# Performance work log

Measured on AMD Instinct MI355X. Metric: run time of the kernel, lower is better.

## Reference

```python
import jax, jax.numpy as jnp
import numpy as np

NEG_SLOPE = 0.2

def gat_conv(x, src, dst, n, W, a_src, a_dst, b):
    # PyG GATConv, heads=1: h = xW; e_ij = LeakyReLU(a_src.h_j + a_dst.h_i)
    # alpha = softmax over incoming edges of i; out_i = sum_j alpha_ij * h_j + b
    h = x @ W                               # [N, F_out]
    s_src = h @ a_src                       # [N]
    s_dst = h @ a_dst                       # [N]
    e = s_src[src] + s_dst[dst]             # [E]
    e = jnp.where(e > 0, e, NEG_SLOPE * e)  # leaky relu
    # numerically stable scatter-softmax over destination groups
    m = jax.ops.segment_max(e, dst, num_segments=n)          # [N]
    ee = jnp.exp(e - m[dst])                                  # [E]
    denom = jax.ops.segment_sum(ee, dst, num_segments=n)      # [N]
    alpha = ee / denom[dst]                                    # [E]
    out = jax.ops.segment_sum(alpha[:, None] * h[src], dst, num_segments=n)
    return out + b

def add_self_loops(edge_index, n):
    loops = jnp.arange(n, dtype=edge_index.dtype)
    src = jnp.concatenate([edge_index[0], loops])
    dst = jnp.concatenate([edge_index[1], loops])
    return src, dst

def setup_inputs() -> dict:
    key = jax.random.key(0)
    ks = jax.random.split(key, 12)
    N, E, F_IN, H1, H2, C = 50000, 800000, 1433, 512, 256, 7
    x = jax.random.normal(ks[0], (N, F_IN), dtype=jnp.float32)
    edge_index = jax.random.randint(ks[1], (2, E), 0, N, dtype=jnp.int64)
    def glorot(k, shape):
        lim = float(np.sqrt(6.0 / (shape[0] + shape[-1])))
        return jax.random.uniform(k, shape, jnp.float32, -lim, lim)
    params = {
        'W1': glorot(ks[2], (F_IN, H1)), 'as1': glorot(ks[3], (H1,)), 'ad1': glorot(ks[4], (H1,)), 'b1': jnp.zeros((H1,), jnp.float32),
        'W2': glorot(ks[5], (H1, H2)), 'as2': glorot(ks[6], (H2,)), 'ad2': glorot(ks[7], (H2,)), 'b2': jnp.zeros((H2,), jnp.float32),
        'W3': glorot(ks[8], (H2, C)), 'as3': glorot(ks[9], (C,)), 'ad3': glorot(ks[10], (C,)), 'b3': jnp.zeros((C,), jnp.float32),
    }
    return {'x': x, 'edge_index': edge_index, **params}

def reference(x, edge_index, W1, as1, ad1, b1, W2, as2, ad2, b2, W3, as3, ad3, b3):
    n = x.shape[0]
    src, dst = add_self_loops(edge_index, n)
    h = jax.nn.relu(gat_conv(x, src, dst, n, W1, as1, ad1, b1))
    h = jax.nn.relu(gat_conv(h, src, dst, n, W2, as2, ad2, b2))
    h = gat_conv(h, src, dst, n, W3, as3, ad3, b3)
    return jax.nn.log_softmax(h, axis=1)
```

## Files before the change

kernel.cpp:

```cpp
#include <hip/hip_runtime.h>
#include <hip/hip_bf16.h>
#include <math.h>

constexpr int N_NODES = 50000;
constexpr int E_EDGES = 800000;
constexpr int E_TOT   = E_EDGES + N_NODES;
constexpr int F_IN  = 1433;
constexpr int KPAD1 = 1440;
constexpr int F1 = 512;
constexpr int F2 = 256;
constexpr int NC = 7;
constexpr int MAXDEG = 1024;
constexpr float NEG_SLOPE = 0.2f;

typedef unsigned short u16;
typedef unsigned int   u32;
typedef short s16x8 __attribute__((ext_vector_type(8)));
typedef float f32x4 __attribute__((ext_vector_type(4)));
typedef float float4a __attribute__((ext_vector_type(4), aligned(4)));

__device__ inline u16 f2b(float f) {
    u32 u = __float_as_uint(f);
    u32 r = (u + 0x7fffu + ((u >> 16) & 1u)) >> 16;
    return (u16)r;
}
__device__ inline float b2f(u16 b) { return __uint_as_float(((u32)b) << 16); }

__device__ inline u32 pkbf16(float lo, float hi) {
    union { __hip_bfloat162 h; u32 u; } c;
    c.h = __float22bfloat162_rn(make_float2(lo, hi));
    return c.u;
}

__device__ inline void gload_lds16(const void* g, void* l) {
    __builtin_amdgcn_global_load_lds(
        (const __attribute__((address_space(1))) u32*)g,
        (__attribute__((address_space(3))) u32*)l, 16, 0, 0);
}

__device__ inline void loadA8_nt(const float* p, int gk, float4a& v0, float4a& v1) {
    if (gk + 8 <= F_IN) {
        v0 = __builtin_nontemporal_load((const float4a*)p);
        v1 = __builtin_nontemporal_load((const float4a*)(p + 4));
    } else {
#pragma unroll
        for (int i = 0; i < 4; ++i) v0[i] = (gk + i < F_IN) ? p[i] : 0.f;
#pragma unroll
        for (int i = 0; i < 4; ++i) v1[i] = (gk + 4 + i < F_IN) ? p[4 + i] : 0.f;
    }
}

__global__ void count_dst_kernel(const int* __restrict__ dst, int* __restrict__ counts) {
    int i = blockIdx.x * blockDim.x + threadIdx.x;
    if (i < E_TOT) {
        int d = (i < E_EDGES) ? dst[i] : (i - E_EDGES);
        atomicAdd(&counts[d], 1);
    }
}

__global__ __launch_bounds__(1024) void scan_kernel(const int* __restrict__ counts,
                                                    int* __restrict__ row_ptr, int n) {
    __shared__ int part[1024];
    int t = threadIdx.x;
    int chunk = (n + 1023) / 1024;
    int lo = t * chunk;
    int hi = min(lo + chunk, n);
    int s = 0;
    for (int i = lo; i < hi; ++i) s += counts[i];
    part[t] = s;
    __syncthreads();
    for (int off = 1; off < 1024; off <<= 1) {
        int v = 0;
        if (t >= off) v = part[t - off];
        __syncthreads();
        part[t] += v;
        __syncthreads();
    }
    int run = part[t] - s;
    for (int i = lo; i < hi; ++i) { row_ptr[i] = run; run += counts[i]; }
    if (t == 1023) row_ptr[n] = part[1023];
}

__global__ void scatter_kernel(const int* __restrict__ src, const int* __restrict__ dst,
                               const int* __restrict__ row_ptr, int* __restrict__ fill,
                               int* __restrict__ col) {
    int i = blockIdx.x * blockDim.x + threadIdx.x;
    if (i < E_TOT) {
        int s = (i < E_EDGES) ? src[i] : (i - E_EDGES);
        int d = (i < E_EDGES) ? dst[i] : (i - E_EDGES);
        int p = row_ptr[d] + atomicAdd(&fill[d], 1);
        col[p] = s;
    }
}

__global__ void convert_wt_kernel(const float* __restrict__ W, u32* __restrict__ Wt,
                                  int K, int Nn, int KP) {
    int p = blockIdx.x * blockDim.x + threadIdx.x;
    int ppr = KP / 2;
    if (p >= Nn * ppr) return;
    int n = p / ppr;
    int k = (p - n * ppr) * 2;
    float v0 = (k + 0 < K) ? W[(size_t)(k + 0) * Nn + n] : 0.f;
    float v1 = (k + 1 < K) ? W[(size_t)(k + 1) * Nn + n] : 0.f;
    Wt[p] = (u32)f2b(v0) | ((u32)f2b(v1) << 16);
}

__global__ __launch_bounds__(256, 2) void gemm1_fused(const float* __restrict__ A,
                                                      const u16* __restrict__ Bt,
                                                      u16* __restrict__ C) {
    constexpr int M = N_NODES;
    constexpr int ABUF = 64 * 32;
    constexpr int BBUF = 512 * 32;
    __shared__ u16 sA[2 * ABUF];
    __shared__ u16 sB[2 * BBUF];
    int tid  = threadIdx.x;
    int wave = tid >> 6;
    int lane = tid & 63;
    int quad = lane >> 4;
    int lm   = lane & 15;
    int m0 = blockIdx.x * 64;

    int arow  = min(m0 + (tid >> 2), M - 1);
    int aslot = (tid & 3) ^ ((tid >> 3) & 3);
    const float* xcol = A + (size_t)arow * F_IN + aslot * 8;
    int acolbase = aslot * 8;

    const u16* gB[8];
    u16* lB[8];
#pragma unroll
    for (int c = 0; c < 8; ++c) {
        int chunk = wave * 8 + c;
        int row  = chunk * 16 + (lane >> 2);
        int slot = (lane & 3) ^ ((lane >> 3) & 3);
        gB[c] = Bt + (size_t)row * KPAD1 + slot * 8;
        lB[c] = &sB[chunk * 512];
    }

    f32x4 acc[4][8];
#pragma unroll
    for (int i = 0; i < 4; ++i)
#pragma unroll
        for (int j = 0; j < 8; ++j) acc[i][j] = (f32x4){0.f, 0.f, 0.f, 0.f};

    int rdoff = (quad ^ ((lm >> 1) & 3)) * 8;

    {
#pragma unroll
        for (int c = 0; c < 8; ++c) gload_lds16(gB[c], lB[c]);
        float4a a0, a1;
        loadA8_nt(xcol, acolbase, a0, a1);
        uint4 pk;
        pk.x = pkbf16(a0[0], a0[1]); pk.y = pkbf16(a0[2], a0[3]);
        pk.z = pkbf16(a1[0], a1[1]); pk.w = pkbf16(a1[2], a1[3]);
        *(uint4*)&sA[tid * 8] = pk;
    }
    __syncthreads();

    int cur = 0;
    for (int k0 = 0; k0 < KPAD1; k0 += 32) {
        int kn = k0 + 32;
        bool hasnext = kn < KPAD1;
        int nxt = cur ^ 1;

        float4a a0, a1;
        if (hasnext) {
#pragma unroll
            for (int c = 0; c < 8; ++c) gload_lds16(gB[c] + kn, lB[c] + nxt * BBUF);
            loadA8_nt(xcol + kn, acolbase + kn, a0, a1);
        }

        const u16* sAc = &sA[cur * ABUF];
        const u16* sBc = &sB[cur * BBUF];
        s16x8 af[4], bf[8];
#pragma unroll
        for (int mt = 0; mt < 4; ++mt)
            af[mt] = *(const s16x8*)&sAc[(mt * 16 + lm) * 32 + rdoff];
#pragma unroll
        for (int nt = 0; nt < 8; ++nt)
            bf[nt] = *(const s16x8*)&sBc[(wave * 128 + nt * 16 + lm) * 32 + rdoff];
#pragma unroll
        for (int mt = 0; mt < 4; ++mt)
#pragma unroll
            for (int nt = 0; nt < 8; ++nt)
                acc[mt][nt] = __builtin_amdgcn_mfma_f32_16x16x32_bf16(
                    af[mt], bf[nt], acc[mt][nt], 0, 0, 0);

        if (hasnext) {
            uint4 pk;
            pk.x = pkbf16(a0[0], a0[1]); pk.y = pkbf16(a0[2], a0[3]);
            pk.z = pkbf16(a1[0], a1[1]); pk.w = pkbf16(a1[2], a1[3]);
            *(uint4*)&sA[nxt * ABUF + tid * 8] = pk;
        }
        __syncthreads();
        cur = nxt;
    }

#pragma unroll
    for (int mt = 0; mt < 4; ++mt) {
        int mbase = m0 + mt * 16 + quad * 4;
#pragma unroll
        for (int nt = 0; nt < 8; ++nt) {
            int n = wave * 128 + nt * 16 + lm;
#pragma unroll
            for (int r = 0; r < 4; ++r) {
                int m = mbase + r;
                if (m < M)
                    __builtin_nontemporal_store(f2b(acc[mt][nt][r]),
                                                &C[(size_t)m * F1 + n]);
            }
        }
    }
}

__global__ __launch_bounds__(256) void mfma_gemm_bt(const u16* __restrict__ A,
                                                    const u16* __restrict__ Bt,
                                                    u16* __restrict__ C,
                                                    int M, int N, int K) {
    __shared__ u16 sA[128 * 32];
    __shared__ u16 sB[128 * 32];
    int tid  = threadIdx.x;
    int wave = tid >> 6;
    int lane = tid & 63;
    int quad = lane >> 4;
    int lm   = lane & 15;
    int wm = wave & 1;
    int wn = wave >> 1;
    int m0 = blockIdx.y * 128;
    int n0 = blockIdx.x * 128;

    int ch0 = wave * 2, ch1 = wave * 2 + 1;
    int rsub = lane >> 2;
    int slot = (lane & 3) ^ ((lane >> 3) & 3);
    int csub = slot * 8;
    int ar0 = min(m0 + ch0 * 16 + rsub, M - 1);
    int ar1 = min(m0 + ch1 * 16 + rsub, M - 1);
    int br0 = n0 + ch0 * 16 + rsub;
    int br1 = n0 + ch1 * 16 + rsub;
    const u16* gA0 = A + (size_t)ar0 * K + csub;
    const u16* gA1 = A + (size_t)ar1 * K + csub;
    const u16* gB0 = Bt + (size_t)br0 * K + csub;
    const u16* gB1 = Bt + (size_t)br1 * K + csub;

    f32x4 acc[4][4];
#pragma unroll
    for (int i = 0; i < 4; ++i)
#pragma unroll
        for (int j = 0; j < 4; ++j) acc[i][j] = (f32x4){0.f, 0.f, 0.f, 0.f};

    int rdoff = (quad ^ ((lm >> 1) & 3)) * 8;

    for (int k0 = 0; k0 < K; k0 += 32) {
        gload_lds16(gA0 + k0, &sA[ch0 * 512]);
        gload_lds16(gA1 + k0, &sA[ch1 * 512]);
        gload_lds16(gB0 + k0, &sB[ch0 * 512]);
        gload_lds16(gB1 + k0, &sB[ch1 * 512]);
        __syncthreads();

        s16x8 af[4], bf[4];
#pragma unroll
        for (int mt = 0; mt < 4; ++mt)
            af[mt] = *(const s16x8*)&sA[(wm * 64 + mt * 16 + lm) * 32 + rdoff];
#pragma unroll
        for (int nt = 0; nt < 4; ++nt)
            bf[nt] = *(const s16x8*)&sB[(wn * 64 + nt * 16 + lm) * 32 + rdoff];
#pragma unroll
        for (int mt = 0; mt < 4; ++mt)
#pragma unroll
            for (int nt = 0; nt < 4; ++nt)
                acc[mt][nt] = __builtin_amdgcn_mfma_f32_16x16x32_bf16(
                    af[mt], bf[nt], acc[mt][nt], 0, 0, 0);
        __syncthreads();
    }

#pragma unroll
    for (int mt = 0; mt < 4; ++mt) {
        int mbase = m0 + wm * 64 + mt * 16 + quad * 4;
#pragma unroll
        for (int nt = 0; nt < 4; ++nt) {
            int n = n0 + wn * 64 + nt * 16 + lm;
#pragma unroll
            for (int r = 0; r < 4; ++r) {
                int m = mbase + r;
                if (m < M) C[(size_t)m * N + n] = f2b(acc[mt][nt][r]);
            }
        }
    }
}

template <int F>
__global__ __launch_bounds__(256) void scores_bf16_kernel(const u16* __restrict__ h,
                                                          const float* __restrict__ a_src,
                                                          const float* __restrict__ a_dst,
                                                          float* __restrict__ s_src,
                                                          float* __restrict__ s_dst, int n) {
    int gwid = (blockIdx.x * blockDim.x + threadIdx.x) >> 6;
    int lane = threadIdx.x & 63;
    if (gwid >= n) return;
    const u32* row = (const u32*)(h + (size_t)gwid * F);
    float acc1 = 0.f, acc2 = 0.f;
    for (int p = lane; p < F / 2; p += 64) {
        u32 u = row[p];
        float v0 = b2f((u16)(u & 0xffff));
        float v1 = b2f((u16)(u >> 16));
        acc1 += v0 * a_src[2 * p] + v1 * a_src[2 * p + 1];
        acc2 += v0 * a_dst[2 * p] + v1 * a_dst[2 * p + 1];
    }
#pragma unroll
    for (int o = 32; o; o >>= 1) {
        acc1 += __shfl_xor(acc1, o);
        acc2 += __shfl_xor(acc2, o);
    }
    if (lane == 0) { s_src[gwid] = acc1; s_dst[gwid] = acc2; }
}

template <int F>
__global__ __launch_bounds__(256) void scores_kernel(const float* __restrict__ h,
                                                     const float* __restrict__ a_src,
                                                     const float* __restrict__ a_dst,
                                                     float* __restrict__ s_src,
                                                     float* __restrict__ s_dst, int n) {
    int gwid = (blockIdx.x * blockDim.x + threadIdx.x) >> 6;
    int lane = threadIdx.x & 63;
    if (gwid >= n) return;
    const float* row = h + (size_t)gwid * F;
    float acc1 = 0.f, acc2 = 0.f;
    for (int f = lane; f < F; f += 64) {
        float v = row[f];
        acc1 += v * a_src[f];
        acc2 += v * a_dst[f];
    }
#pragma unroll
    for (int o = 32; o; o >>= 1) {
        acc1 += __shfl_xor(acc1, o);
        acc2 += __shfl_xor(acc2, o);
    }
    if (lane == 0) { s_src[gwid] = acc1; s_dst[gwid] = acc2; }
}

template <int F, bool OUT_BF16>
__global__ __launch_bounds__(256) void agg_online_kernel(
        const u16* __restrict__ h, const float* __restrict__ s_src,
        const float* __restrict__ s_dst, const float* __restrict__ bias,
        const int* __restrict__ row_ptr, const int* __restrict__ col,
        void* __restrict__ out, int n) {
    constexpr int UPL = F / 128;
    int gwid = (blockIdx.x * blockDim.x + threadIdx.x) >> 6;
    int lane = threadIdx.x & 63;
    if (gwid >= n) return;
    int beg = row_ptr[gwid];
    int end = row_ptr[gwid + 1];
    float sd = s_dst[gwid];
    const u32* hw = (const u32*)h;
    int loff = lane * UPL;

    float m = -1e30f, denom = 0.f;
    float acc[2 * UPL];
#pragma unroll
    for (int e = 0; e < 2 * UPL; ++e) acc[e] = 0.f;

    int j = beg;
    for (; j + 2 <= end; j += 2) {
        int c0 = col[j], c1 = col[j + 1];
        const u32* r0 = hw + (size_t)c0 * (F / 2) + loff;
        const u32* r1 = hw + (size_t)c1 * (F / 2) + loff;
        u32 v0[UPL], v1[UPL];
        if constexpr (UPL == 4) {
            uint4 q0 = *(const uint4*)r0; v0[0]=q0.x; v0[1]=q0.y; v0[2]=q0.z; v0[3]=q0.w;
            uint4 q1 = *(const uint4*)r1; v1[0]=q1.x; v1[1]=q1.y; v1[2]=q1.z; v1[3]=q1.w;
        } else {
            uint2 q0 = *(const uint2*)r0; v0[0]=q0.x; v0[1]=q0.y;
            uint2 q1 = *(const uint2*)r1; v1[0]=q1.x; v1[1]=q1.y;
        }
        float e0 = s_src[c0] + sd; e0 = (e0 > 0.f) ? e0 : NEG_SLOPE * e0;
        float e1 = s_src[c1] + sd; e1 = (e1 > 0.f) ? e1 : NEG_SLOPE * e1;
        float mn = fmaxf(fmaxf(m, e0), e1);
        float sc = expf(m - mn);
        float w0 = expf(e0 - mn);
        float w1 = expf(e1 - mn);
        denom = denom * sc + w0 + w1;
        m = mn;
#pragma unroll
        for (int u = 0; u < UPL; ++u) {
            acc[2*u]   = acc[2*u]   * sc + w0 * b2f((u16)(v0[u] & 0xffff))
                                         + w1 * b2f((u16)(v1[u] & 0xffff));
            acc[2*u+1] = acc[2*u+1] * sc + w0 * b2f((u16)(v0[u] >> 16))
                                         + w1 * b2f((u16)(v1[u] >> 16));
        }
    }
    if (j < end) {
        int c0 = col[j];
        const u32* r0 = hw + (size_t)c0 * (F / 2) + loff;
        u32 v0[UPL];
        if constexpr (UPL == 4) {
            uint4 q0 = *(const uint4*)r0; v0[0]=q0.x; v0[1]=q0.y; v0[2]=q0.z; v0[3]=q0.w;
        } else {
            uint2 q0 = *(const uint2*)r0; v0[0]=q0.x; v0[1]=q0.y;
        }
        float e0 = s_src[c0] + sd; e0 = (e0 > 0.f) ? e0 : NEG_SLOPE * e0;
        float mn = fmaxf(m, e0);
        float sc = expf(m - mn);
        float w0 = expf(e0 - mn);
        denom = denom * sc + w0;
        m = mn;
#pragma unroll
        for (int u = 0; u < UPL; ++u) {
            acc[2*u]   = acc[2*u]   * sc + w0 * b2f((u16)(v0[u] & 0xffff));
            acc[2*u+1] = acc[2*u+1] * sc + w0 * b2f((u16)(v0[u] >> 16));
        }
    }

    float inv = 1.0f / denom;
    if constexpr (OUT_BF16) {
        const float2* bp2 = (const float2*)bias;
        u32 ov[UPL];
#pragma unroll
        for (int u = 0; u < UPL; ++u) {
            float2 bb = bp2[loff + u];
            float v0 = fmaxf(acc[2*u]   * inv + bb.x, 0.f);
            float v1 = fmaxf(acc[2*u+1] * inv + bb.y, 0.f);
            ov[u] = pkbf16(v0, v1);
        }
        u32* op = (u32*)out + (size_t)gwid * (F / 2) + loff;
        if constexpr (UPL == 4) {
            uint4 q = {ov[0], ov[1], ov[2], ov[3]};
            *(uint4*)op = q;
        } else {
            uint2 q = {ov[0], ov[1]};
            *(uint2*)op = q;
        }
    } else {
        const float* bp = bias + 2 * loff;
        float4 q = { fmaxf(acc[0] * inv + bp[0], 0.f),
                     fmaxf(acc[1] * inv + bp[1], 0.f),
                     fmaxf(acc[2] * inv + bp[2], 0.f),
                     fmaxf(acc[3] * inv + bp[3], 0.f) };
        *(float4*)((float*)out + (size_t)gwid * F + 2 * loff) = q;
    }
}

__global__ __launch_bounds__(64) void agg_lsm7_kernel(const float* __restrict__ h,
                                                      const float* __restrict__ s_src,
                                                      const float* __restrict__ s_dst,
                                                      const float* __restrict__ bias,
                                                      const int* __restrict__ row_ptr,
                                                      const int* __restrict__ col,
                                                      float* __restrict__ out) {
    int node = blockIdx.x;
    int lane = threadIdx.x;
    int beg = row_ptr[node];
    int deg = min(row_ptr[node + 1] - beg, MAXDEG);

    __shared__ float w[MAXDEG];
    __shared__ int cs[MAXDEG];

    float sd = s_dst[node];
    float m = -1e30f;
    for (int j = lane; j < deg; j += 64) {
        int s = col[beg + j];
        cs[j] = s;
        float e = s_src[s] + sd;
        e = (e > 0.f) ? e : NEG_SLOPE * e;
        w[j] = e;
        m = fmaxf(m, e);
    }
#pragma unroll
    for (int o = 32; o; o >>= 1) m = fmaxf(m, __shfl_xor(m, o));
    float sum = 0.f;
    for (int j = lane; j < deg; j += 64) {
        float v = expf(w[j] - m);
        w[j] = v;
        sum += v;
    }
#pragma unroll
    for (int o = 32; o; o >>= 1) sum += __shfl_xor(sum, o);
    float inv = 1.0f / sum;

    float a[NC];
#pragma unroll
    for (int f = 0; f < NC; ++f) a[f] = 0.f;
    for (int j = lane; j < deg; j += 64) {
        float wg = w[j] * inv;
        const float* row = h + (size_t)cs[j] * NC;
#pragma unroll
        for (int f = 0; f < NC; ++f) a[f] += wg * row[f];
    }
#pragma unroll
    for (int f = 0; f < NC; ++f)
#pragma unroll
        for (int o = 32; o; o >>= 1) a[f] += __shfl_xor(a[f], o);

    if (lane == 0) {
        float vals[NC];
        float mx = -1e30f;
#pragma unroll
        for (int f = 0; f < NC; ++f) { vals[f] = a[f] + bias[f]; mx = fmaxf(mx, vals[f]); }
        float ssum = 0.f;
#pragma unroll
        for (int f = 0; f < NC; ++f) ssum += expf(vals[f] - mx);
        float lse = mx + logf(ssum);
#pragma unroll
        for (int f = 0; f < NC; ++f) out[(size_t)node * NC + f] = vals[f] - lse;
    }
}

__global__ __launch_bounds__(256) void gemm3_kernel(const float* __restrict__ A,
                                                    const float* __restrict__ W,
                                                    float* __restrict__ out, int n) {
    __shared__ float sW[F2 * NC];
    for (int i = threadIdx.x; i < F2 * NC; i += blockDim.x) sW[i] = W[i];
    __syncthreads();
    int gwid = (blockIdx.x * blockDim.x + threadIdx.x) >> 6;
    int lane = threadIdx.x & 63;
    if (gwid >= n) return;
    const float* row = A + (size_t)gwid * F2;
    float4 v = *(const float4*)(row + lane * 4);
    float res = 0.f;
#pragma unroll
    for (int c = 0; c < NC; ++c) {
        float p = v.x * sW[(lane * 4 + 0) * NC + c] + v.y * sW[(lane * 4 + 1) * NC + c] +
                  v.z * sW[(lane * 4 + 2) * NC + c] + v.w * sW[(lane * 4 + 3) * NC + c];
#pragma unroll
        for (int o = 32; o; o >>= 1) p += __shfl_xor(p, o);
        if (lane == c) res = p;
    }
    if (lane < NC) out[(size_t)gwid * NC + lane] = res;
}

extern "C" void kernel_launch(void* const* d_in, const int* in_sizes, int n_in,
                              void* d_out, int out_size, void* d_ws, size_t ws_size,
                              hipStream_t stream) {
    const float* x   = (const float*)d_in[0];
    const int* ei    = (const int*)d_in[1];
    const int* src   = ei;
    const int* dst   = ei + E_EDGES;
    const float* W1  = (const float*)d_in[2];
    const float* as1 = (const float*)d_in[3];
    const float* ad1 = (const float*)d_in[4];
    const float* b1  = (const float*)d_in[5];
    const float* W2  = (const float*)d_in[6];
    const float* as2 = (const float*)d_in[7];
    const float* ad2 = (const float*)d_in[8];
    const float* b2  = (const float*)d_in[9];
    const float* W3  = (const float*)d_in[10];
    const float* as3 = (const float*)d_in[11];
    const float* ad3 = (const float*)d_in[12];
    const float* b3  = (const float*)d_in[13];
    float* outp = (float*)d_out;

    char* base = (char*)d_ws;
    u16*  a1b = (u16*)base;
    u16*  h2b = (u16*)(base + 51200000);
    float* a2 = (float*)(base + 76800000);
    float* h3 = (float*)(base + 128000000);
    u16*  h1b = (u16*)(base + 144000000);
    u16*  W1t = (u16*)(base + 195200000);
    u16*  W2t = (u16*)(base + 196674560);
    float* ssrc = (float*)(base + 196936704);
    float* sdst = (float*)(base + 197136704);
    int* row_ptr = (int*)(base + 197336704);
    int* counts  = (int*)(base + 197536708);
    int* fill    = (int*)(base + 197736708);
    int* col     = (int*)(base + 197936708);

    hipMemsetAsync(counts, 0, sizeof(int) * N_NODES, stream);
    hipMemsetAsync(fill, 0, sizeof(int) * N_NODES, stream);

    {
        int blk = 256;
        int grid = (E_TOT + blk - 1) / blk;
        count_dst_kernel<<<grid, blk, 0, stream>>>(dst, counts);
        scan_kernel<<<1, 1024, 0, stream>>>(counts, row_ptr, N_NODES);
        scatter_kernel<<<grid, blk, 0, stream>>>(src, dst, row_ptr, fill, col);
    }

    {
        int nw1 = F1 * (KPAD1 / 2);
        convert_wt_kernel<<<(nw1 + 255) / 256, 256, 0, stream>>>(W1, (u32*)W1t, F_IN, F1, KPAD1);
        int nw2 = F2 * (F1 / 2);
        convert_wt_kernel<<<(nw2 + 255) / 256, 256, 0, stream>>>(W2, (u32*)W2t, F1, F2, F1);
    }

    int waves_grid = (N_NODES + 3) / 4;
    int mblocks = (N_NODES + 127) / 128;

    {
        int grid1 = (N_NODES + 63) / 64;
        gemm1_fused<<<grid1, 256, 0, stream>>>(x, W1t, h1b);
        scores_bf16_kernel<F1><<<waves_grid, 256, 0, stream>>>(h1b, as1, ad1, ssrc, sdst, N_NODES);
        agg_online_kernel<F1, true><<<waves_grid, 256, 0, stream>>>(
            h1b, ssrc, sdst, b1, row_ptr, col, a1b, N_NODES);
    }
    {
        dim3 grid(F2 / 128, mblocks);
        mfma_gemm_bt<<<grid, 256, 0, stream>>>(a1b, W2t, h2b, N_NODES, F2, F1);
        scores_bf16_kernel<F2><<<waves_grid, 256, 0, stream>>>(h2b, as2, ad2, ssrc, sdst, N_NODES);
        agg_online_kernel<F2, false><<<waves_grid, 256, 0, stream>>>(
            h2b, ssrc, sdst, b2, row_ptr, col, a2, N_NODES);
    }
    {
        gemm3_kernel<<<waves_grid, 256, 0, stream>>>(a2, W3, h3, N_NODES);
        scores_kernel<NC><<<waves_grid, 256, 0, stream>>>(h3, as3, ad3, ssrc, sdst, N_NODES);
        agg_lsm7_kernel<<<N_NODES, 64, 0, stream>>>(
            h3, ssrc, sdst, b3, row_ptr, col, outp);
    }
}
```

Baseline: 1.056 ms.

## Fuse attention score dot-products into GEMM epilogues and use online-softmax final aggregation

Computes s_src/s_dst inside each layer's GEMM epilogue from the fp32 accumulators, which removes the separate scores kernels and their re-read of h. Layer 2 spans two column blocks, so it accumulates partial scores with atomics into buffers zeroed by memsets. The final 7-class aggregation becomes a one-wave-per-node online-softmax kernel with no shared-memory degree cap. The nontemporal loads and stores in gemm1 are also replaced with regular ones, which changes cache behaviour, and scores now come from fp32 accumulators rather than rounded bf16 values.

```diff
diff --git a/kernel.cpp b/kernel.cpp
--- a/kernel.cpp
+++ b/kernel.cpp
@@ -10,7 +10,6 @@
 constexpr int F1 = 512;
 constexpr int F2 = 256;
 constexpr int NC = 7;
-constexpr int MAXDEG = 1024;
 constexpr float NEG_SLOPE = 0.2f;
 
 typedef unsigned short u16;
@@ -38,10 +37,10 @@
         (__attribute__((address_space(3))) u32*)l, 16, 0, 0);
 }
 
-__device__ inline void loadA8_nt(const float* p, int gk, float4a& v0, float4a& v1) {
+__device__ inline void loadA8(const float* p, int gk, float4a& v0, float4a& v1) {
     if (gk + 8 <= F_IN) {
-        v0 = __builtin_nontemporal_load((const float4a*)p);
-        v1 = __builtin_nontemporal_load((const float4a*)(p + 4));
+        v0 = *(const float4a*)p;
+        v1 = *(const float4a*)(p + 4);
     } else {
 #pragma unroll
         for (int i = 0; i < 4; ++i) v0[i] = (gk + i < F_IN) ? p[i] : 0.f;
@@ -107,12 +106,17 @@
 
 __global__ __launch_bounds__(256, 2) void gemm1_fused(const float* __restrict__ A,
                                                       const u16* __restrict__ Bt,
-                                                      u16* __restrict__ C) {
+                                                      u16* __restrict__ C,
+                                                      const float* __restrict__ a_src,
+                                                      const float* __restrict__ a_dst,
+                                                      float* __restrict__ s_src,
+                                                      float* __restrict__ s_dst) {
     constexpr int M = N_NODES;
     constexpr int ABUF = 64 * 32;
     constexpr int BBUF = 512 * 32;
     __shared__ u16 sA[2 * ABUF];
     __shared__ u16 sB[2 * BBUF];
+    __shared__ float sRed[4][64][2];
     int tid  = threadIdx.x;
     int wave = tid >> 6;
     int lane = tid & 63;
@@ -148,7 +152,7 @@
 #pragma unroll
         for (int c = 0; c < 8; ++c) gload_lds16(gB[c], lB[c]);
         float4a a0, a1;
-        loadA8_nt(xcol, acolbase, a0, a1);
+        loadA8(xcol, acolbase, a0, a1);
         uint4 pk;
         pk.x = pkbf16(a0[0], a0[1]); pk.y = pkbf16(a0[2], a0[3]);
         pk.z = pkbf16(a1[0], a1[1]); pk.w = pkbf16(a1[2], a1[3]);
@@ -166,7 +170,7 @@
         if (hasnext) {
 #pragma unroll
             for (int c = 0; c < 8; ++c) gload_lds16(gB[c] + kn, lB[c] + nxt * BBUF);
-            loadA8_nt(xcol + kn, acolbase + kn, a0, a1);
+            loadA8(xcol + kn, acolbase + kn, a0, a1);
         }
 
         const u16* sAc = &sA[cur * ABUF];
@@ -204,10 +208,45 @@
 #pragma unroll
             for (int r = 0; r < 4; ++r) {
                 int m = mbase + r;
-                if (m < M)
-                    __builtin_nontemporal_store(f2b(acc[mt][nt][r]),
-                                                &C[(size_t)m * F1 + n]);
-            }
+                if (m < M) C[(size_t)m * F1 + n] = f2b(acc[mt][nt][r]);
+            }
+        }
+    }
+
+    float asn[8], adn[8];
+#pragma unroll
+    for (int nt = 0; nt < 8; ++nt) {
+        int n = wave * 128 + nt * 16 + lm;
+        asn[nt] = a_src[n];
+        adn[nt] = a_dst[n];
+    }
+#pragma unroll
+    for (int mt = 0; mt < 4; ++mt)
+#pragma unroll
+        for (int r = 0; r < 4; ++r) {
+            float ps = 0.f, pd = 0.f;
+#pragma unroll
+            for (int nt = 0; nt < 8; ++nt) {
+                ps += acc[mt][nt][r] * asn[nt];
+                pd += acc[mt][nt][r] * adn[nt];
+            }
+#pragma unroll
+            for (int o = 1; o < 16; o <<= 1) {
+                ps += __shfl_xor(ps, o);
+                pd += __shfl_xor(pd, o);
+            }
+            if (lm == 0) {
+                int mloc = mt * 16 + quad * 4 + r;
+                sRed[wave][mloc][0] = ps;
+                sRed[wave][mloc][1] = pd;
+            }
+        }
+    __syncthreads();
+    if (tid < 64) {
+        int m = m0 + tid;
+        if (m < M) {
+            s_src[m] = sRed[0][tid][0] + sRed[1][tid][0] + sRed[2][tid][0] + sRed[3][tid][0];
+            s_dst[m] = sRed[0][tid][1] + sRed[1][tid][1] + sRed[2][tid][1] + sRed[3][tid][1];
         }
     }
 }
@@ -215,9 +254,14 @@
 __global__ __launch_bounds__(256) void mfma_gemm_bt(const u16* __restrict__ A,
                                                     const u16* __restrict__ Bt,
                                                     u16* __restrict__ C,
-                                                    int M, int N, int K) {
+                                                    int M, int N, int K,
+                                                    const float* __restrict__ a_src,
+                                                    const float* __restrict__ a_dst,
+                                                    float* __restrict__ s_src,
+                                                    float* __restrict__ s_dst) {
     __shared__ u16 sA[128 * 32];
     __shared__ u16 sB[128 * 32];
+    __shared__ float sRed[2][2][64][2];
     int tid  = threadIdx.x;
     int wave = tid >> 6;
     int lane = tid & 63;
@@ -285,56 +329,44 @@
             }
         }
     }
-}
-
-template <int F>
-__global__ __launch_bounds__(256) void scores_bf16_kernel(const u16* __restrict__ h,
-                                                          const float* __restrict__ a_src,
-                                                          const float* __restrict__ a_dst,
-                                                          float* __restrict__ s_src,
-                                                          float* __restrict__ s_dst, int n) {
-    int gwid = (blockIdx.x * blockDim.x + threadIdx.x) >> 6;
-    int lane = threadIdx.x & 63;
-    if (gwid >= n) return;
-    const u32* row = (const u32*)(h + (size_t)gwid * F);
-    float acc1 = 0.f, acc2 = 0.f;
-    for (int p = lane; p < F / 2; p += 64) {
-        u32 u = row[p];
-        float v0 = b2f((u16)(u & 0xffff));
-        float v1 = b2f((u16)(u >> 16));
-        acc1 += v0 * a_src[2 * p] + v1 * a_src[2 * p + 1];
-        acc2 += v0 * a_dst[2 * p] + v1 * a_dst[2 * p + 1];
-    }
-#pragma unroll
-    for (int o = 32; o; o >>= 1) {
-        acc1 += __shfl_xor(acc1, o);
-        acc2 += __shfl_xor(acc2, o);
-    }
-    if (lane == 0) { s_src[gwid] = acc1; s_dst[gwid] = acc2; }
-}
-
-template <int F>
-__global__ __launch_bounds__(256) void scores_kernel(const float* __restrict__ h,
-                                                     const float* __restrict__ a_src,
-                                                     const float* __restrict__ a_dst,
-                                                     float* __restrict__ s_src,
-                                                     float* __restrict__ s_dst, int n) {
-    int gwid = (blockIdx.x * blockDim.x + threadIdx.x) >> 6;
-    int lane = threadIdx.x & 63;
-    if (gwid >= n) return;
-    const float* row = h + (size_t)gwid * F;
-    float acc1 = 0.f, acc2 = 0.f;
-    for (int f = lane; f < F; f += 64) {
-        float v = row[f];
-        acc1 += v * a_src[f];
-        acc2 += v * a_dst[f];
-    }
-#pragma unroll
-    for (int o = 32; o; o >>= 1) {
-        acc1 += __shfl_xor(acc1, o);
-        acc2 += __shfl_xor(acc2, o);
-    }
-    if (lane == 0) { s_src[gwid] = acc1; s_dst[gwid] = acc2; }
+
+    float asn[4], adn[4];
+#pragma unroll
+    for (int nt = 0; nt < 4; ++nt) {
+        int n = n0 + wn * 64 + nt * 16 + lm;
+        asn[nt] = a_src[n];
+        adn[nt] = a_dst[n];
+    }
+#pragma unroll
+    for (int mt = 0; mt < 4; ++mt)
+#pragma unroll
+        for (int r = 0; r < 4; ++r) {
+            float ps = 0.f, pd = 0.f;
+#pragma unroll
+            for (int nt = 0; nt < 4; ++nt) {
+                ps += acc[mt][nt][r] * asn[nt];
+                pd += acc[mt][nt][r] * adn[nt];
+            }
+#pragma unroll
+            for (int o = 1; o < 16; o <<= 1) {
+                ps += __shfl_xor(ps, o);
+                pd += __shfl_xor(pd, o);
+            }
+            if (lm == 0) {
+                int mloc = mt * 16 + quad * 4 + r;
+                sRed[wm][wn][mloc][0] = ps;
+                sRed[wm][wn][mloc][1] = pd;
+            }
+        }
+    __syncthreads();
+    if (tid < 128) {
+        int wmf = tid >> 6, mloc = tid & 63;
+        int m = m0 + wmf * 64 + mloc;
+        if (m < M) {
+            atomicAdd(&s_src[m], sRed[wmf][0][mloc][0] + sRed[wmf][1][mloc][0]);
+            atomicAdd(&s_dst[m], sRed[wmf][0][mloc][1] + sRed[wmf][1][mloc][1]);
+        }
+    }
 }
 
 template <int F, bool OUT_BF16>
@@ -438,74 +470,79 @@
     }
 }
 
-__global__ __launch_bounds__(64) void agg_lsm7_kernel(const float* __restrict__ h,
-                                                      const float* __restrict__ s_src,
-                                                      const float* __restrict__ s_dst,
-                                                      const float* __restrict__ bias,
-                                                      const int* __restrict__ row_ptr,
-                                                      const int* __restrict__ col,
-                                                      float* __restrict__ out) {
-    int node = blockIdx.x;
-    int lane = threadIdx.x;
-    int beg = row_ptr[node];
-    int deg = min(row_ptr[node + 1] - beg, MAXDEG);
-
-    __shared__ float w[MAXDEG];
-    __shared__ int cs[MAXDEG];
-
-    float sd = s_dst[node];
-    float m = -1e30f;
-    for (int j = lane; j < deg; j += 64) {
-        int s = col[beg + j];
-        cs[j] = s;
-        float e = s_src[s] + sd;
+__global__ __launch_bounds__(256) void agg_lsm7_kernel(const float* __restrict__ h,
+                                                       const float* __restrict__ s_src,
+                                                       const float* __restrict__ s_dst,
+                                                       const float* __restrict__ bias,
+                                                       const int* __restrict__ row_ptr,
+                                                       const int* __restrict__ col,
+                                                       float* __restrict__ out, int n) {
+    int gwid = (blockIdx.x * blockDim.x + threadIdx.x) >> 6;
+    int lane = threadIdx.x & 63;
+    if (gwid >= n) return;
+    int beg = row_ptr[gwid];
+    int end = row_ptr[gwid + 1];
+    float sd = s_dst[gwid];
+
+    float m = -1e30f, denom = 0.f;
+    float a[NC];
+#pragma unroll
+    for (int f = 0; f < NC; ++f) a[f] = 0.f;
+
+    for (int j = beg + lane; j < end; j += 64) {
+        int c = col[j];
+        float e = s_src[c] + sd;
         e = (e > 0.f) ? e : NEG_SLOPE * e;
-        w[j] = e;
-        m = fmaxf(m, e);
-    }
-#pragma unroll
-    for (int o = 32; o; o >>= 1) m = fmaxf(m, __shfl_xor(m, o));
-    float sum = 0.f;
-    for (int j = lane; j < deg; j += 64) {
-        float v = expf(w[j] - m);
-        w[j] = v;
-        sum += v;
-    }
-#pragma unroll
-    for (int o = 32; o; o >>= 1) sum += __shfl_xor(sum, o);
-    float inv = 1.0f / sum;
-
-    float a[NC];
-#pragma unroll
-    for (int f = 0; f < NC; ++f) a[f] = 0.f;
-    for (int j = lane; j < deg; j += 64) {
-        float wg = w[j] * inv;
-        const float* row = h + (size_t)cs[j] * NC;
-#pragma unroll
-        for (int f = 0; f < NC; ++f) a[f] += wg * row[f];
-    }
-#pragma unroll
-    for (int f = 0; f < NC; ++f)
-#pragma unroll
-        for (int o = 32; o; o >>= 1) a[f] += __shfl_xor(a[f], o);
+        float mn = fmaxf(m, e);
+        float sc = expf(m - mn);
+        float w = expf(e - mn);
+        denom = denom * sc + w;
+        m = mn;
+        const float* hr = h + (size_t)c * NC;
+#pragma unroll
+        for (int f = 0; f < NC; ++f) a[f] = a[f] * sc + w * hr[f];
+    }
+#pragma unroll
+    for (int o = 32; o; o >>= 1) {
+        float mo = __shfl_xor(m, o);
+        float dn = __shfl_xor(denom, o);
+        float M2 = fmaxf(m, mo);
+        float s1 = expf(m - M2);
+        float s2 = expf(mo - M2);
+        denom = denom * s1 + dn * s2;
+#pragma unroll
+        for (int f = 0; f < NC; ++f) {
+            float af = __shfl_xor(a[f], o);
+            a[f] = a[f] * s1 + af * s2;
+        }
+        m = M2;
+    }
 
     if (lane == 0) {
+        float inv = 1.0f / denom;
         float vals[NC];
         float mx = -1e30f;
 #pragma unroll
-        for (int f = 0; f < NC; ++f) { vals[f] = a[f] + bias[f]; mx = fmaxf(mx, vals[f]); }
+        for (int f = 0; f < NC; ++f) {
+            vals[f] = a[f] * inv + bias[f];
+            mx = fmaxf(mx, vals[f]);
+        }
         float ssum = 0.f;
 #pragma unroll
         for (int f = 0; f < NC; ++f) ssum += expf(vals[f] - mx);
         float lse = mx + logf(ssum);
 #pragma unroll
-        for (int f = 0; f < NC; ++f) out[(size_t)node * NC + f] = vals[f] - lse;
+        for (int f = 0; f < NC; ++f) out[(size_t)gwid * NC + f] = vals[f] - lse;
     }
 }
 
 __global__ __launch_bounds__(256) void gemm3_kernel(const float* __restrict__ A,
                                                     const float* __restrict__ W,
-                                                    float* __restrict__ out, int n) {
+                                                    float* __restrict__ out, int n,
+                                                    const float* __restrict__ a_src,
+                                                    const float* __restrict__ a_dst,
+                                                    float* __restrict__ s_src,
+                                                    float* __restrict__ s_dst) {
     __shared__ float sW[F2 * NC];
     for (int i = threadIdx.x; i < F2 * NC; i += blockDim.x) sW[i] = W[i];
     __syncthreads();
@@ -524,6 +561,14 @@
         if (lane == c) res = p;
     }
     if (lane < NC) out[(size_t)gwid * NC + lane] = res;
+    float p1 = (lane < NC) ? res * a_src[lane] : 0.f;
+    float p2 = (lane < NC) ? res * a_dst[lane] : 0.f;
+#pragma unroll
+    for (int o = 1; o < 8; o <<= 1) {
+        p1 += __shfl_xor(p1, o);
+        p2 += __shfl_xor(p2, o);
+    }
+    if (lane == 0) { s_src[gwid] = p1; s_dst[gwid] = p2; }
 }
 
 extern "C" void kernel_launch(void* const* d_in, const int* in_sizes, int n_in,
@@ -585,22 +630,23 @@
 
     {
         int grid1 = (N_NODES + 63) / 64;
-        gemm1_fused<<<grid1, 256, 0, stream>>>(x, W1t, h1b);
-        scores_bf16_kernel<F1><<<waves_grid, 256, 0, stream>>>(h1b, as1, ad1, ssrc, sdst, N_NODES);
+        gemm1_fused<<<grid1, 256, 0, stream>>>(x, W1t, h1b, as1, ad1, ssrc, sdst);
         agg_online_kernel<F1, true><<<waves_grid, 256, 0, stream>>>(
             h1b, ssrc, sdst, b1, row_ptr, col, a1b, N_NODES);
     }
     {
+        hipMemsetAsync(ssrc, 0, sizeof(float) * N_NODES, stream);
+        hipMemsetAsync(sdst, 0, sizeof(float) * N_NODES, stream);
         dim3 grid(F2 / 128, mblocks);
-        mfma_gemm_bt<<<grid, 256, 0, stream>>>(a1b, W2t, h2b, N_NODES, F2, F1);
-        scores_bf16_kernel<F2><<<waves_grid, 256, 0, stream>>>(h2b, as2, ad2, ssrc, sdst, N_NODES);
+        mfma_gemm_bt<<<grid, 256, 0, stream>>>(a1b, W2t, h2b, N_NODES, F2, F1,
+                                               as2, ad2, ssrc, sdst);
         agg_online_kernel<F2, false><<<waves_grid, 256, 0, stream>>>(
             h2b, ssrc, sdst, b2, row_ptr, col, a2, N_NODES);
     }
     {
-        gemm3_kernel<<<waves_grid, 256, 0, stream>>>(a2, W3, h3, N_NODES);
-        scores_kernel<NC><<<waves_grid, 256, 0, stream>>>(h3, as3, ad3, ssrc, sdst, N_NODES);
-        agg_lsm7_kernel<<<N_NODES, 64, 0, stream>>>(
-            h3, ssrc, sdst, b3, row_ptr, col, outp);
-    }
-}
+        gemm3_kernel<<<waves_grid, 256, 0, stream>>>(a2, W3, h3, N_NODES,
+                                                     as3, ad3, ssrc, sdst);
+        agg_lsm7_kernel<<<waves_grid, 256, 0, stream>>>(
+            h3, ssrc, sdst, b3, row_ptr, col, outp, N_NODES);
+    }
+}
```

New measurement: 991.1 us. -6.1%, faster.
